# Kernel tuning notes

Measured on AMD Instinct MI355X. Metric: run time of the kernel, lower is better.

The kernel has to match this reference:

```python
import jax, jax.numpy as jnp
import numpy as np

THRESHOLD = 0.5
MAX_POINTS = 10000
NORMALIZE = True
BIDIRECTIONAL = True
INF = jnp.float32(1e30)


def _voxels_to_points(vox):
    # vox: (D, H, W). Returns padded points (MAX_POINTS, 3) and validity mask.
    D, H, W = vox.shape
    flat = vox.reshape(-1)
    active = flat > THRESHOLD
    n_active = jnp.sum(active.astype(jnp.int32))
    # Stable argsort puts active voxel indices first (deterministic stand-in
    # for torch's randperm subsampling when n_active > MAX_POINTS).
    order = jnp.argsort(jnp.where(active, 0, 1).astype(jnp.int32))
    idx = order[:MAX_POINTS]
    valid = jnp.arange(MAX_POINTS) < jnp.minimum(n_active, MAX_POINTS)
    d = idx // (H * W)
    h = (idx // W) % H
    w = idx % W
    pts = jnp.stack([d, h, w], axis=-1).astype(jnp.float32)  # (MAX_POINTS, 3)
    if NORMALIZE:
        pts = pts / (D - 1) * 2.0 - 1.0
    pts = jnp.where(valid[:, None], pts, 0.0)
    return pts, valid


def _chamfer_single(p1, v1, p2, v2):
    # p1: (N,3), p2: (M,3) padded; v1/v2 are validity masks.
    n1 = jnp.sum(p1 * p1, axis=1)  # (N,)
    n2 = jnp.sum(p2 * p2, axis=1)  # (M,)
    dist = n1[:, None] + n2[None, :] - 2.0 * (p1 @ p2.T)  # (N, M)
    dist = jnp.maximum(dist, 0.0)
    c1 = jnp.maximum(jnp.sum(v1.astype(jnp.float32)), 1.0)
    c2 = jnp.maximum(jnp.sum(v2.astype(jnp.float32)), 1.0)
    min_1to2 = jnp.min(jnp.where(v2[None, :], dist, INF), axis=1)  # (N,)
    loss = jnp.sum(jnp.where(v1, min_1to2, 0.0)) / c1
    if BIDIRECTIONAL:
        min_2to1 = jnp.min(jnp.where(v1[:, None], dist, INF), axis=0)  # (M,)
        loss = loss + jnp.sum(jnp.where(v2, min_2to1, 0.0)) / c2
    return loss


def setup_inputs() -> dict:
    key = jax.random.key(0)
    k1, k2 = jax.random.split(key)
    pred = jax.random.uniform(k1, (4, 1, 64, 64, 64), dtype=jnp.float32)
    target = jax.random.uniform(k2, (4, 1, 64, 64, 64), dtype=jnp.float32)
    return {"pred": pred, "target": target}


def reference(pred, target):
    B = pred.shape[0]
    total = jnp.float32(0.0)
    n_valid = jnp.float32(0.0)
    for b in range(B):  # small fixed batch loop (per-sample dist matrix is 10k x 10k)
        p1, v1 = _voxels_to_points(pred[b, 0])
        p2, v2 = _voxels_to_points(target[b, 0])
        has_pts = jnp.logical_and(jnp.any(v1), jnp.any(v2))
        cd = _chamfer_single(p1, v1, p2, v2)
        total = total + jnp.where(has_pts, cd, 0.0)
        n_valid = n_valid + has_pts.astype(jnp.float32)
    return jnp.where(n_valid > 0, total / jnp.maximum(n_valid, 1.0), 0.0)
```

## Files before the change

### kernel.cpp

```cpp
#include <hip/hip_runtime.h>
#include <hip/hip_bf16.h>


#define NVOX      262144
#define NCHUNK    256
#define MAXPTS    10000
#define PTS_PAD   10240
#define NCLOUD    8
#define NTASK     8
#define NRB       40
#define QPW       160
#define QPB       640
#define NQB       16
#define RSPLIT    8
#define RLEN      1280
#define RSTEPS    40
#define SCALE     (2.0f/63.0f)

typedef _Float16 half8  __attribute__((ext_vector_type(8)));
typedef float    f32x16 __attribute__((ext_vector_type(16)));

#define WS_TOTALS   0
#define WS_COUNTS   1024
#define WS_OFFSETS  16384
#define WS_QFRAG    32768
#define WS_RFRAG    1343488
#define WS_NQ       2654208
#define WS_SMIN     2981888
#define WS_BSUM     5603328

__device__ __forceinline__ const float* cloud_src(const float* pred, const float* tgt, int cloud) {
    const float* base = (cloud & 1) ? tgt : pred;
    return base + (size_t)(cloud >> 1) * NVOX;
}

__global__ void k_count(const float* __restrict__ pred, const float* __restrict__ tgt,
                        int* __restrict__ counts,
                        half8* __restrict__ Qfrag, half8* __restrict__ Rfrag,
                        float* __restrict__ nqint) {
    int gi = blockIdx.x * 256 + threadIdx.x;
    if (gi < NCLOUD * PTS_PAD) {
        half8 zq = {0, 0, 0, 0, 0, 0, 0, 0};
        half8 zr = {0, 0, 0, (_Float16)4096, 0, 0, 0, 0};
        Qfrag[gi] = zq;
        Rfrag[gi] = zr;
        nqint[gi] = 0.f;
    }
    int cloud = blockIdx.x >> 8;
    int chunk = blockIdx.x & 255;
    int t = threadIdx.x;
    const float* src = cloud_src(pred, tgt, cloud) + chunk * 1024;
    float4 v = reinterpret_cast<const float4*>(src)[t];
    int cnt = (v.x > 0.5f) + (v.y > 0.5f) + (v.z > 0.5f) + (v.w > 0.5f);
    __shared__ int s[256];
    s[t] = cnt; __syncthreads();
    for (int o = 128; o > 0; o >>= 1) {
        if (t < o) s[t] += s[t + o];
        __syncthreads();
    }
    if (t == 0) counts[cloud * NCHUNK + chunk] = s[0];
}

__global__ void k_scan(const int* __restrict__ counts, int* __restrict__ offsets,
                       int* __restrict__ totals) {
    int cloud = blockIdx.x;
    int t = threadIdx.x;
    int c = counts[cloud * NCHUNK + t];
    __shared__ int s[256];
    s[t] = c; __syncthreads();
    for (int o = 1; o < 256; o <<= 1) {
        int v = (t >= o) ? s[t - o] : 0;
        __syncthreads();
        s[t] += v;
        __syncthreads();
    }
    offsets[cloud * NCHUNK + t] = s[t] - c;
    if (t == 255) totals[cloud] = s[255];
}

__global__ void k_compact(const float* __restrict__ pred, const float* __restrict__ tgt,
                          const int* __restrict__ offsets,
                          half8* __restrict__ Qfrag, half8* __restrict__ Rfrag,
                          float* __restrict__ nqint) {
    int cloud = blockIdx.x >> 8;
    int chunk = blockIdx.x & 255;
    int t = threadIdx.x;
    const float* src = cloud_src(pred, tgt, cloud) + chunk * 1024;
    float4 v = reinterpret_cast<const float4*>(src)[t];
    int f0 = v.x > 0.5f, f1 = v.y > 0.5f, f2 = v.z > 0.5f, f3 = v.w > 0.5f;
    int cnt = f0 + f1 + f2 + f3;
    __shared__ int s[256];
    s[t] = cnt; __syncthreads();
    for (int o = 1; o < 256; o <<= 1) {
        int x = (t >= o) ? s[t - o] : 0;
        __syncthreads();
        s[t] += x;
        __syncthreads();
    }
    int rank = offsets[cloud * NCHUNK + chunk] + (s[t] - cnt);
    int eidx = chunk * 1024 + t * 4;
    int flags[4] = {f0, f1, f2, f3};
    size_t base = (size_t)cloud * PTS_PAD;
    #pragma unroll
    for (int e = 0; e < 4; ++e) {
        if (flags[e]) {
            if (rank < MAXPTS) {
                int idx = eidx + e;
                int d = idx >> 12, h = (idx >> 6) & 63, w = idx & 63;
                int nr = d * d + h * h + w * w;
                half8 Q = {(_Float16)(-2 * d), (_Float16)(-2 * h), (_Float16)(-2 * w),
                           (_Float16)8, (_Float16)1, 0, 0, 0};
                half8 R = {(_Float16)d, (_Float16)h, (_Float16)w,
                           (_Float16)(nr >> 3), (_Float16)(nr & 7), 0, 0, 0};
                Qfrag[base + rank] = Q;
                Rfrag[base + rank] = R;
                nqint[base + rank] = (float)nr;
            }
            rank++;
        }
    }
}

__device__ __forceinline__ float red16(f32x16 d, float m) {
    float t0 = fminf(fminf(d[0], d[1]), d[2]);
    float t1 = fminf(fminf(d[3], d[4]), d[5]);
    float t2 = fminf(fminf(d[6], d[7]), d[8]);
    float t3 = fminf(fminf(d[9], d[10]), d[11]);
    float t4 = fminf(fminf(d[12], d[13]), d[14]);
    float t5 = fminf(d[15], m);
    float u0 = fminf(fminf(t0, t1), t2);
    float u1 = fminf(fminf(t3, t4), t5);
    return fminf(u0, u1);
}

#define SB __builtin_amdgcn_sched_barrier(0)

#define MM(dd, aa, bb)                                                         \
    asm("v_mfma_f32_32x32x16_f16 %0, %1, %2, 0"                                \
        : "=&v"(dd) : "v"(aa), "v"(bb));                                       \
    SB
#define MMP(dd, aa, bb)                                                        \
    asm("v_mfma_f32_32x32x16_f16 %0, %1, %2, 0\n\t"                            \
        "s_nop 7\n\ts_nop 7\n\ts_nop 7"                                        \
        : "=&v"(dd) : "v"(aa), "v"(bb));                                       \
    SB

#define BODY(areg)                                                             \
    do {                                                                       \
        f32x16 d0_, d1_, d2_, d3_, d4_;                                        \
        MM(d0_, areg, bq0);                                                    \
        MMP(d1_, areg, bq1);                                                   \
        m0 = red16(d0_, m0); SB;                                               \
        MM(d2_, areg, bq2);                                                    \
        m1 = red16(d1_, m1); SB;                                               \
        MM(d3_, areg, bq3);                                                    \
        m2 = red16(d2_, m2); SB;                                               \
        MMP(d4_, areg, bq4);                                                   \
        m3 = red16(d3_, m3); SB;                                               \
        m4 = red16(d4_, m4); SB;                                               \
    } while (0)

__global__ __launch_bounds__(256, 4) void k_chamfer(const half8* __restrict__ Qfrag,
                                                    const half8* __restrict__ Rfrag,
                                                    float* __restrict__ smin) {
    int task = blockIdx.x >> 7;
    int rem  = blockIdx.x & 127;
    int qb   = rem >> 3;
    int rs   = rem & 7;
    int b = task >> 1, dir = task & 1;
    int qc = 2 * b + dir;
    int rc = 2 * b + (dir ^ 1);
    int tid = threadIdx.x, wave = tid >> 6, lane = tid & 63;
    int l32 = lane & 31;

    int qbase = qb * QPB + wave * QPW;
    half8 zero8 = {0, 0, 0, 0, 0, 0, 0, 0};
    half8 bq0 = zero8, bq1 = zero8, bq2 = zero8, bq3 = zero8, bq4 = zero8;
    if (lane < 32) {
        const half8* qp = Qfrag + (size_t)qc * PTS_PAD + qbase + l32;
        bq0 = qp[0]; bq1 = qp[32]; bq2 = qp[64]; bq3 = qp[96]; bq4 = qp[128];
    }
    float m0 = 1e30f, m1 = 1e30f, m2 = 1e30f, m3 = 1e30f, m4 = 1e30f;

    const half8* rp0 = Rfrag + (size_t)rc * PTS_PAD + rs * RLEN + l32;
    half8 a = rp0[0];
    half8 an = rp0[32];

    #pragma unroll 1
    for (int t = 0; t < RSTEPS - 2; ++t) {
        half8 a2 = rp0[32 * t + 64];
        BODY(a);
        a = an;
        an = a2;
    }
    BODY(a);
    BODY(an);

    m0 = fminf(m0, __shfl_xor(m0, 32));
    m1 = fminf(m1, __shfl_xor(m1, 32));
    m2 = fminf(m2, __shfl_xor(m2, 32));
    m3 = fminf(m3, __shfl_xor(m3, 32));
    m4 = fminf(m4, __shfl_xor(m4, 32));
    if (lane < 32) {
        float* outp = smin + ((size_t)task * RSPLIT + rs) * PTS_PAD + qbase + l32;
        outp[0]   = m0;
        outp[32]  = m1;
        outp[64]  = m2;
        outp[96]  = m3;
        outp[128] = m4;
    }
}

__global__ void k_reduce(const float* __restrict__ nqint, const int* __restrict__ totals,
                         const float* __restrict__ smin, float* __restrict__ bsum) {
    int task = blockIdx.x / NRB;
    int rb   = blockIdx.x % NRB;
    int tid  = threadIdx.x;
    int qi   = rb * 256 + tid;
    int qc   = 2 * (task >> 1) + (task & 1);
    int countQ = min(totals[qc], MAXPTS);

    const float SC2 = SCALE * SCALE;
    float contrib = 0.f;
    if (qi < countQ) {
        const float* s = smin + (size_t)task * RSPLIT * PTS_PAD + qi;
        float mn = fminf(fminf(s[0 * PTS_PAD], s[1 * PTS_PAD]),
                         fminf(s[2 * PTS_PAD], s[3 * PTS_PAD]));
        mn = fminf(mn, fminf(fminf(s[4 * PTS_PAD], s[5 * PTS_PAD]),
                             fminf(s[6 * PTS_PAD], s[7 * PTS_PAD])));
        float nq = nqint[(size_t)qc * PTS_PAD + qi];
        contrib = fmaxf((nq + mn) * SC2, 0.f);
    }
    __shared__ float sb[256];
    sb[tid] = contrib; __syncthreads();
    for (int o = 128; o > 0; o >>= 1) {
        if (tid < o) sb[tid] += sb[tid + o];
        __syncthreads();
    }
    if (tid == 0) bsum[task * NRB + rb] = sb[0];
}

__global__ void k_final(const float* __restrict__ bsum, const int* __restrict__ totals,
                        float* __restrict__ out) {
    int t = threadIdx.x;
    __shared__ float sh[NTASK];
    if (t < NTASK) {
        float s = 0.f;
        #pragma unroll
        for (int i = 0; i < NRB; ++i) s += bsum[t * NRB + i];
        sh[t] = s;
    }
    __syncthreads();
    if (t == 0) {
        float total = 0.f, nv = 0.f;
        for (int b = 0; b < 4; ++b) {
            int c1 = min(totals[2 * b], MAXPTS);
            int c2 = min(totals[2 * b + 1], MAXPTS);
            float cd = sh[2 * b] / fmaxf((float)c1, 1.f) + sh[2 * b + 1] / fmaxf((float)c2, 1.f);
            if (c1 > 0 && c2 > 0) { total += cd; nv += 1.f; }
        }
        out[0] = (nv > 0.f) ? total / nv : 0.f;
    }
}

extern "C" void kernel_launch(void* const* d_in, const int* in_sizes, int n_in,
                              void* d_out, int out_size, void* d_ws, size_t ws_size,
                              hipStream_t stream) {
    const float* pred = (const float*)d_in[0];
    const float* tgt  = (const float*)d_in[1];
    float* out = (float*)d_out;

    char* ws = (char*)d_ws;
    int*   totals  = (int*)(ws + WS_TOTALS);
    int*   counts  = (int*)(ws + WS_COUNTS);
    int*   offsets = (int*)(ws + WS_OFFSETS);
    half8* Qfrag   = (half8*)(ws + WS_QFRAG);
    half8* Rfrag   = (half8*)(ws + WS_RFRAG);
    float* nqint   = (float*)(ws + WS_NQ);
    float* smin    = (float*)(ws + WS_SMIN);
    float* bsum    = (float*)(ws + WS_BSUM);

    k_count  <<<NCLOUD * NCHUNK, 256, 0, stream>>>(pred, tgt, counts, Qfrag, Rfrag, nqint);
    k_scan   <<<NCLOUD,          256, 0, stream>>>(counts, offsets, totals);
    k_compact<<<NCLOUD * NCHUNK, 256, 0, stream>>>(pred, tgt, offsets, Qfrag, Rfrag, nqint);
    k_chamfer<<<NTASK * NQB * RSPLIT, 256, 0, stream>>>(Qfrag, Rfrag, smin);
    k_reduce <<<NTASK * NRB,     256, 0, stream>>>(nqint, totals, smin, bsum);
    k_final  <<<1, 64, 0, stream>>>(bsum, totals, out);
}
```

Before: 54.05 us.

## Retile chamfer kernel to fewer queries per wave and drop inline-asm MFMA scheduling

Reduces each wave's query tile from 160 to 64 points (two MFMA accumulators instead of five). It halves the reference split from 8 to 4, so each block scans 2560 reference points, and raises the block count and launch-bounds occupancy hint. The hand-scheduled inline-asm MFMA sequence with s_nop padding and sched barriers is replaced by compiler builtins, and the reduce kernel now merges 4 partial minima instead of 8. Each wave now has less independent MFMA work to hide latency, and reference fragments are reused across fewer queries, which raises load traffic per MFMA. In exchange the compiler gets more freedom to schedule and occupancy may be higher.

```diff
diff --git a/kernel.cpp b/kernel.cpp
--- a/kernel.cpp
+++ b/kernel.cpp
@@ -9,12 +9,12 @@
 #define NCLOUD    8
 #define NTASK     8
 #define NRB       40
-#define QPW       160
-#define QPB       640
-#define NQB       16
-#define RSPLIT    8
-#define RLEN      1280
-#define RSTEPS    40
+#define QPW       64
+#define QPB       256
+#define NQB       40
+#define RSPLIT    4
+#define RLEN      2560
+#define RSTEPS    80
 #define SCALE     (2.0f/63.0f)
 
 typedef _Float16 half8  __attribute__((ext_vector_type(8)));
@@ -27,7 +27,7 @@
 #define WS_RFRAG    1343488
 #define WS_NQ       2654208
 #define WS_SMIN     2981888
-#define WS_BSUM     5603328
+#define WS_BSUM     4292608
 
 __device__ __forceinline__ const float* cloud_src(const float* pred, const float* tgt, int cloud) {
     const float* base = (cloud & 1) ? tgt : pred;
@@ -133,40 +133,13 @@
     return fminf(u0, u1);
 }
 
-#define SB __builtin_amdgcn_sched_barrier(0)
-
-#define MM(dd, aa, bb)                                                         \
-    asm("v_mfma_f32_32x32x16_f16 %0, %1, %2, 0"                                \
-        : "=&v"(dd) : "v"(aa), "v"(bb));                                       \
-    SB
-#define MMP(dd, aa, bb)                                                        \
-    asm("v_mfma_f32_32x32x16_f16 %0, %1, %2, 0\n\t"                            \
-        "s_nop 7\n\ts_nop 7\n\ts_nop 7"                                        \
-        : "=&v"(dd) : "v"(aa), "v"(bb));                                       \
-    SB
-
-#define BODY(areg)                                                             \
-    do {                                                                       \
-        f32x16 d0_, d1_, d2_, d3_, d4_;                                        \
-        MM(d0_, areg, bq0);                                                    \
-        MMP(d1_, areg, bq1);                                                   \
-        m0 = red16(d0_, m0); SB;                                               \
-        MM(d2_, areg, bq2);                                                    \
-        m1 = red16(d1_, m1); SB;                                               \
-        MM(d3_, areg, bq3);                                                    \
-        m2 = red16(d2_, m2); SB;                                               \
-        MMP(d4_, areg, bq4);                                                   \
-        m3 = red16(d3_, m3); SB;                                               \
-        m4 = red16(d4_, m4); SB;                                               \
-    } while (0)
-
-__global__ __launch_bounds__(256, 4) void k_chamfer(const half8* __restrict__ Qfrag,
+__global__ __launch_bounds__(256, 5) void k_chamfer(const half8* __restrict__ Qfrag,
                                                     const half8* __restrict__ Rfrag,
                                                     float* __restrict__ smin) {
-    int task = blockIdx.x >> 7;
-    int rem  = blockIdx.x & 127;
-    int qb   = rem >> 3;
-    int rs   = rem & 7;
+    int task = blockIdx.x / (NQB * RSPLIT);
+    int rem  = blockIdx.x % (NQB * RSPLIT);
+    int qb   = rem / RSPLIT;
+    int rs   = rem % RSPLIT;
     int b = task >> 1, dir = task & 1;
     int qc = 2 * b + dir;
     int rc = 2 * b + (dir ^ 1);
@@ -175,39 +148,46 @@
 
     int qbase = qb * QPB + wave * QPW;
     half8 zero8 = {0, 0, 0, 0, 0, 0, 0, 0};
-    half8 bq0 = zero8, bq1 = zero8, bq2 = zero8, bq3 = zero8, bq4 = zero8;
+    half8 bq0 = zero8, bq1 = zero8;
     if (lane < 32) {
         const half8* qp = Qfrag + (size_t)qc * PTS_PAD + qbase + l32;
-        bq0 = qp[0]; bq1 = qp[32]; bq2 = qp[64]; bq3 = qp[96]; bq4 = qp[128];
-    }
-    float m0 = 1e30f, m1 = 1e30f, m2 = 1e30f, m3 = 1e30f, m4 = 1e30f;
+        bq0 = qp[0]; bq1 = qp[32];
+    }
+    float m0 = 1e30f, m1 = 1e30f;
+    f32x16 cz;
+    #pragma unroll
+    for (int e = 0; e < 16; ++e) cz[e] = 0.f;
 
     const half8* rp0 = Rfrag + (size_t)rc * PTS_PAD + rs * RLEN + l32;
-    half8 a = rp0[0];
+    half8 a  = rp0[0];
     half8 an = rp0[32];
 
-    #pragma unroll 1
     for (int t = 0; t < RSTEPS - 2; ++t) {
         half8 a2 = rp0[32 * t + 64];
-        BODY(a);
+        f32x16 d0 = __builtin_amdgcn_mfma_f32_32x32x16_f16(a, bq0, cz, 0, 0, 0);
+        f32x16 d1 = __builtin_amdgcn_mfma_f32_32x32x16_f16(a, bq1, cz, 0, 0, 0);
+        m0 = red16(d0, m0);
+        m1 = red16(d1, m1);
         a = an;
         an = a2;
     }
-    BODY(a);
-    BODY(an);
+    {
+        f32x16 d0 = __builtin_amdgcn_mfma_f32_32x32x16_f16(a, bq0, cz, 0, 0, 0);
+        f32x16 d1 = __builtin_amdgcn_mfma_f32_32x32x16_f16(a, bq1, cz, 0, 0, 0);
+        m0 = red16(d0, m0);
+        m1 = red16(d1, m1);
+        d0 = __builtin_amdgcn_mfma_f32_32x32x16_f16(an, bq0, cz, 0, 0, 0);
+        d1 = __builtin_amdgcn_mfma_f32_32x32x16_f16(an, bq1, cz, 0, 0, 0);
+        m0 = red16(d0, m0);
+        m1 = red16(d1, m1);
+    }
 
     m0 = fminf(m0, __shfl_xor(m0, 32));
     m1 = fminf(m1, __shfl_xor(m1, 32));
-    m2 = fminf(m2, __shfl_xor(m2, 32));
-    m3 = fminf(m3, __shfl_xor(m3, 32));
-    m4 = fminf(m4, __shfl_xor(m4, 32));
     if (lane < 32) {
         float* outp = smin + ((size_t)task * RSPLIT + rs) * PTS_PAD + qbase + l32;
-        outp[0]   = m0;
-        outp[32]  = m1;
-        outp[64]  = m2;
-        outp[96]  = m3;
-        outp[128] = m4;
+        outp[0]  = m0;
+        outp[32] = m1;
     }
 }
 
@@ -226,8 +206,6 @@
         const float* s = smin + (size_t)task * RSPLIT * PTS_PAD + qi;
         float mn = fminf(fminf(s[0 * PTS_PAD], s[1 * PTS_PAD]),
                          fminf(s[2 * PTS_PAD], s[3 * PTS_PAD]));
-        mn = fminf(mn, fminf(fminf(s[4 * PTS_PAD], s[5 * PTS_PAD]),
-                             fminf(s[6 * PTS_PAD], s[7 * PTS_PAD])));
         float nq = nqint[(size_t)qc * PTS_PAD + qi];
         contrib = fmaxf((nq + mn) * SC2, 0.f);
     }
```

Result: faster. 50.67 us (-6.3%).
